# Performance work log

Hardware: AMD Instinct MI355X
Metric: run time of the kernel (lower is better)

## Reference

```python
import jax, jax.numpy as jnp
import numpy as np

B, T, D, H = 4, 2048, 1024, 16
DK, DV, K, I = 48, 96, 4, 3072
EPS = 1e-5


def rmsnorm(x, w, eps=EPS):
    return x * jax.lax.rsqrt(jnp.mean(x * x, -1, keepdims=True) + eps) * w


def l2norm(x, eps=1e-6):
    return x * jax.lax.rsqrt(jnp.sum(x * x, -1, keepdims=True) + eps)


def causal_conv(x, w):
    # x: [B,T,C], w: [C,K]; causal depthwise conv (torch cross-correlation semantics)
    k = w.shape[1]
    xp = jnp.pad(x, ((0, 0), (k - 1, 0), (0, 0))).transpose(0, 2, 1)  # [B,C,T+K-1]
    y = jax.lax.conv_general_dilated(xp, w[:, None, :], (1,), 'VALID',
                                     feature_group_count=w.shape[0])
    return y.transpose(0, 2, 1)


def gated_delta_rule(q, k, v, g, beta):
    # q,k: [B,T,H,DK]  v: [B,T,H,DV]  g,beta: [B,T,H]
    scale = q.shape[-1] ** -0.5
    qT = jnp.moveaxis(q, 1, 0) * scale
    kT = jnp.moveaxis(k, 1, 0)
    vT = jnp.moveaxis(v, 1, 0)
    gT = jnp.moveaxis(g, 1, 0)
    bT = jnp.moveaxis(beta, 1, 0)
    S0 = jnp.zeros((q.shape[0], q.shape[2], q.shape[3], v.shape[3]), q.dtype)

    def step(S, inp):
        q_t, k_t, v_t, g_t, b_t = inp
        S = S * jnp.exp(g_t)[..., None, None]                      # gated decay
        v_new = (v_t - jnp.einsum('bhk,bhkv->bhv', k_t, S)) * b_t[..., None]
        S = S + k_t[..., None] * v_new[..., None, :]               # delta-rule update
        o_t = jnp.einsum('bhk,bhkv->bhv', q_t, S)
        return S, o_t

    _, o = jax.lax.scan(step, S0, (qT, kT, vT, gT, bT))
    return jnp.moveaxis(o, 0, 1)


def setup_inputs() -> dict:
    key = jax.random.key(0)
    ks = jax.random.split(key, 20)
    s = 0.02
    return {
        'hidden_states': jax.random.normal(ks[0], (B, T, D), jnp.float32),
        'norm1_w': jnp.ones((D,), jnp.float32),
        'q_w': jax.random.normal(ks[1], (D, H * DK), jnp.float32) * s,
        'k_w': jax.random.normal(ks[2], (D, H * DK), jnp.float32) * s,
        'v_w': jax.random.normal(ks[3], (D, H * DV), jnp.float32) * s,
        'conv_q_w': jax.random.normal(ks[4], (H * DK, K), jnp.float32) * 0.2,
        'conv_k_w': jax.random.normal(ks[5], (H * DK, K), jnp.float32) * 0.2,
        'conv_v_w': jax.random.normal(ks[6], (H * DV, K), jnp.float32) * 0.2,
        'b_w': jax.random.normal(ks[7], (D, H), jnp.float32) * s,
        'a_w': jax.random.normal(ks[8], (D, H), jnp.float32) * s,
        'A_log': jnp.log(jax.random.uniform(ks[9], (H,), jnp.float32, 1.0, 16.0)),
        'dt_bias': jax.random.normal(ks[10], (H,), jnp.float32) * 0.5,
        'g_w': jax.random.normal(ks[11], (D, H * DV), jnp.float32) * s,
        'o_norm_w': jnp.ones((DV,), jnp.float32),
        'o_w': jax.random.normal(ks[12], (H * DV, D), jnp.float32) * s,
        'norm2_w': jnp.ones((D,), jnp.float32),
        'gate_w': jax.random.normal(ks[13], (D, I), jnp.float32) * s,
        'up_w': jax.random.normal(ks[14], (D, I), jnp.float32) * s,
        'down_w': jax.random.normal(ks[15], (I, D), jnp.float32) * s,
    }


def reference(hidden_states, norm1_w, q_w, k_w, v_w, conv_q_w, conv_k_w, conv_v_w,
              b_w, a_w, A_log, dt_bias, g_w, o_norm_w, o_w, norm2_w,
              gate_w, up_w, down_w):
    x = hidden_states
    h = rmsnorm(x, norm1_w)
    # --- GatedDeltaNet mixer ---
    q = jax.nn.silu(causal_conv(h @ q_w, conv_q_w)).reshape(B, T, H, DK)
    k = jax.nn.silu(causal_conv(h @ k_w, conv_k_w)).reshape(B, T, H, DK)
    v = jax.nn.silu(causal_conv(h @ v_w, conv_v_w)).reshape(B, T, H, DV)
    q, k = l2norm(q), l2norm(k)
    beta = jax.nn.sigmoid(h @ b_w)                                  # [B,T,H]
    g = -jnp.exp(A_log) * jax.nn.softplus(h @ a_w + dt_bias)        # [B,T,H] mamba gate
    o = gated_delta_rule(q, k, v, g, beta)                          # [B,T,H,DV]
    gate = (h @ g_w).reshape(B, T, H, DV)
    o = rmsnorm(o, o_norm_w) * (gate * jax.nn.sigmoid(gate))        # fused gated RMSNorm
    x = x + o.reshape(B, T, H * DV) @ o_w
    # --- SwiGLU MLP ---
    h2 = rmsnorm(x, norm2_w)
    x = x + (jax.nn.silu(h2 @ gate_w) * (h2 @ up_w)) @ down_w
    return x
```

## Files before the change

### kernel.cpp

```cpp
#include <hip/hip_runtime.h>
#include <hip/hip_bf16.h>
#include <math.h>

constexpr int Bn = 4, Tn = 2048, Dn = 1024, Hn = 16, DKn = 48, DVn = 96, In = 3072;
constexpr int BT = Bn * Tn;
constexpr int HDK = Hn * DKn;
constexpr int HDV = Hn * DVn;
constexpr int QKVC = 2 * HDK + HDV;
constexpr int CC = 64;
constexpr int NC = Tn / CC;

using bf16 = __hip_bfloat16;
typedef __attribute__((ext_vector_type(8))) short bf16x8;
typedef __attribute__((ext_vector_type(4))) float f32x4;

constexpr size_t WO_HBF   = 0;
constexpr size_t WO_QKVR  = 16777216;
constexpr size_t WO_OSC   = 16777216;
constexpr size_t WO_ACT   = 16777216;
constexpr size_t WO_A     = 16777216;
constexpr size_t WO_B     = 26214400;
constexpr size_t WO_ST    = 45088768;
constexpr size_t WO_QKVC  = 67108864;
constexpr size_t WO_GATE  = 117440512;
constexpr size_t WO_X1    = 142606336;
constexpr size_t WO_BA    = 176160768;
constexpr size_t WO_GC    = 177209344;
constexpr size_t WO_T     = 177733632;
constexpr size_t WO_UV    = 194510848;
constexpr size_t WO_WB    = 219676672;
constexpr size_t WB_QKVT = 0;
constexpr size_t WB_GT   = 3145728;
constexpr size_t WB_OT   = 4718592;
constexpr size_t WB_GATET= 6291456;
constexpr size_t WB_UPT  = 9437184;
constexpr size_t WB_DOWNT= 12582912;
constexpr size_t WB_ABT  = 15728640;

__device__ __forceinline__ float sigmoidf_(float x) { return 1.f / (1.f + __expf(-x)); }
__device__ __forceinline__ float siluf(float x) { return x * sigmoidf_(x); }

__device__ __forceinline__ void glds16(const void* g, void* l) {
  __builtin_amdgcn_global_load_lds((const __attribute__((address_space(1))) void*)g,
                                   (__attribute__((address_space(3))) void*)l, 16, 0, 0);
}

__device__ __forceinline__ f32x4 mfma16(bf16x8 a, bf16x8 b, f32x4 c) {
  return __builtin_amdgcn_mfma_f32_16x16x32_bf16(a, b, c, 0, 0, 0);
}

__device__ __forceinline__ bf16x8 scale8(bf16x8 a, float s) {
  bf16x8 r;
#pragma unroll
  for (int e = 0; e < 8; e++) {
    float f = __bfloat162float(__ushort_as_bfloat16((unsigned short)a[e])) * s;
    r[e] = (short)__bfloat16_as_ushort(__float2bfloat16(f));
  }
  return r;
}

__device__ __forceinline__ float b2f(short u) {
  return __bfloat162float(__ushort_as_bfloat16((unsigned short)u));
}
__device__ __forceinline__ short f2b(float f) {
  return (short)__bfloat16_as_ushort(__float2bfloat16(f));
}

struct TcastArgs {
  const float* src[10];
  bf16* dst[10];
  int R[10], C[10], gxw[10], t0[10];
};

__global__ void tcast_all(TcastArgs a) {
  __shared__ float t[32][33];
  int bid = blockIdx.x;
  int i = 0;
#pragma unroll
  for (int k = 1; k < 10; k++) if (bid >= a.t0[k]) i = k;
  int lt = bid - a.t0[i];
  int gxw = a.gxw[i];
  int bx = lt % gxw, by = lt / gxw;
  const float* in = a.src[i];
  bf16* out = a.dst[i];
  int R = a.R[i], C = a.C[i];
  int tx = threadIdx.x, ty = threadIdx.y;
  int c0 = bx * 32, r0 = by * 32;
#pragma unroll
  for (int j = 0; j < 4; j++) {
    int r = ty + j * 8;
    float v = (c0 + tx < C) ? in[(size_t)(r0 + r) * C + c0 + tx] : 0.f;
    t[r][tx] = v;
  }
  __syncthreads();
#pragma unroll
  for (int j = 0; j < 4; j++) {
    int cc = ty + j * 8;
    if (c0 + cc < C) out[(size_t)(c0 + cc) * R + r0 + tx] = __float2bfloat16(t[tx][cc]);
  }
}

__global__ void rmsnorm_bf_k(const float* __restrict__ x, const float* __restrict__ w,
                             bf16* __restrict__ y) {
  int row = blockIdx.x;
  const float4* xr = (const float4*)(x + (size_t)row * Dn);
  int tid = threadIdx.x;
  float4 v = xr[tid];
  float ss = v.x * v.x + v.y * v.y + v.z * v.z + v.w * v.w;
  for (int m = 32; m >= 1; m >>= 1) ss += __shfl_xor(ss, m, 64);
  __shared__ float wsum[4];
  if ((tid & 63) == 0) wsum[tid >> 6] = ss;
  __syncthreads();
  ss = wsum[0] + wsum[1] + wsum[2] + wsum[3];
  float rs = rsqrtf(ss * (1.f / Dn) + 1e-5f);
  float4 wv = ((const float4*)w)[tid];
  bf16* yr = y + (size_t)row * Dn + tid * 4;
  yr[0] = __float2bfloat16(v.x * rs * wv.x);
  yr[1] = __float2bfloat16(v.y * rs * wv.y);
  yr[2] = __float2bfloat16(v.z * rs * wv.z);
  yr[3] = __float2bfloat16(v.w * rs * wv.w);
}

#define AS256(bi) (lds + (bi) * 8192)
#define BS256(bi) (lds + 32768 + (bi) * 8192)
#define STAGE256(bi, k0) do { \
    glds16(gA0 + (k0), AS256(bi) + w * 512); \
    glds16(gB0 + (k0), BS256(bi) + w * 512); \
  } while (0)

__global__ __launch_bounds__(1024) void gemm256(
    const bf16* __restrict__ A, const bf16* __restrict__ Bt,
    bf16* __restrict__ C0, bf16* __restrict__ C1,
    int gx, int N, int K, int mode) {
  __shared__ bf16 lds[65536];
  int bid = blockIdx.x;
  int xcd = bid & 7, li = bid >> 3;
  int by = xcd * 4 + li / gx;
  int bx = li % gx;
  int bm = by * 256, bn = bx * 256;
  int tid = threadIdx.x;
  int lane = tid & 63, w = tid >> 6;
  int l15 = lane & 15, lq = lane >> 4;
  int wr = w >> 2, wc = w & 3;
  int arow0 = tid >> 2;
  int srcq = (tid & 3) ^ ((arow0 >> 1) & 3);
  const bf16* gA0 = A + (size_t)(bm + arow0) * K + srcq * 8;
  const bf16* gB0 = Bt + (size_t)(bn + arow0) * K + srcq * 8;
  int slot = lq ^ ((l15 >> 1) & 3);
  f32x4 acc[4][4];
#pragma unroll
  for (int m = 0; m < 4; m++)
#pragma unroll
    for (int n = 0; n < 4; n++) acc[m][n] = (f32x4){0.f, 0.f, 0.f, 0.f};
  int NT = K >> 5;
  STAGE256(0, 0);
  STAGE256(1, 32);
  STAGE256(2, 64);
  for (int t = 0; t < NT; ++t) {
    int b = t & 3;
    if (t <= NT - 3)      { asm volatile("s_waitcnt vmcnt(4)" ::: "memory"); }
    else if (t == NT - 2) { asm volatile("s_waitcnt vmcnt(2)" ::: "memory"); }
    else                  { asm volatile("s_waitcnt vmcnt(0)" ::: "memory"); }
    __builtin_amdgcn_s_barrier();
    bf16x8 af[4], bfr[4];
#pragma unroll
    for (int m = 0; m < 4; m++)
      af[m] = *(const bf16x8*)(AS256(b) + (wr * 64 + m * 16 + l15) * 32 + slot * 8);
#pragma unroll
    for (int n = 0; n < 4; n++)
      bfr[n] = *(const bf16x8*)(BS256(b) + (wc * 64 + n * 16 + l15) * 32 + slot * 8);
    __builtin_amdgcn_s_setprio(1);
#pragma unroll
    for (int m = 0; m < 4; m++)
#pragma unroll
      for (int n = 0; n < 4; n++)
        acc[m][n] = mfma16(af[m], bfr[n], acc[m][n]);
    __builtin_amdgcn_s_setprio(0);
    if (t + 3 < NT) STAGE256((t + 3) & 3, (t + 3) * 32);
  }
  __syncthreads();
  bf16* dst; int ldc, bnl;
  if (bn < 3072) { dst = C0; ldc = 3072; bnl = bn; }
  else           { dst = C1; ldc = 1536; bnl = bn - 3072; }
  bf16* cw = lds + w * 4096;
#pragma unroll
  for (int m = 0; m < 4; m++)
#pragma unroll
    for (int n = 0; n < 4; n++)
#pragma unroll
      for (int i = 0; i < 4; i++) {
        int row_l = m * 16 + lq * 4 + i;
        int col_l = n * 16 + l15;
        cw[row_l * 64 + (col_l ^ ((row_l & 7) << 3))] = __float2bfloat16(acc[m][n][i]);
      }
  __syncthreads();
  int r8 = lane >> 3, cblk = lane & 7;
#pragma unroll
  for (int it = 0; it < 8; it++) {
    int row_l = it * 8 + r8;
    int sblk = cblk ^ (row_l & 7);
    bf16x8 val = *(const bf16x8*)&cw[row_l * 64 + sblk * 8];
    *(bf16x8*)&dst[(size_t)(bm + wr * 64 + row_l) * ldc + bnl + wc * 64 + cblk * 8] = val;
  }
}

__global__ __launch_bounds__(1024) void gemm_mlp(
    const bf16* __restrict__ A, const bf16* __restrict__ Bt,
    bf16* __restrict__ C, int K) {
  __shared__ bf16 lds[65536];
  int bid = blockIdx.x;
  int xcd = bid & 7, li = bid >> 3;
  int by = xcd * 4 + li / 24;
  int bx = li % 24;
  int bm = by * 256, bn = bx * 128;
  int tid = threadIdx.x;
  int lane = tid & 63, w = tid >> 6;
  int l15 = lane & 15, lq = lane >> 4;
  int wr = w >> 2, wc = w & 3;
  int r0 = tid >> 2;
  int srcq = (tid & 3) ^ ((r0 >> 1) & 3);
  const bf16* gA0 = A + (size_t)(bm + r0) * K + srcq * 8;
  int growB = bn + (r0 & 127) + (r0 >> 7) * 3072;
  const bf16* gB0 = Bt + (size_t)growB * K + srcq * 8;
  int slot = lq ^ ((l15 >> 1) & 3);
  f32x4 accg[4][2], accu[4][2];
#pragma unroll
  for (int m = 0; m < 4; m++)
#pragma unroll
    for (int n = 0; n < 2; n++) {
      accg[m][n] = (f32x4){0.f, 0.f, 0.f, 0.f};
      accu[m][n] = (f32x4){0.f, 0.f, 0.f, 0.f};
    }
  int NT = K >> 5;
  STAGE256(0, 0);
  STAGE256(1, 32);
  STAGE256(2, 64);
  for (int t = 0; t < NT; ++t) {
    int b = t & 3;
    if (t <= NT - 3)      { asm volatile("s_waitcnt vmcnt(4)" ::: "memory"); }
    else if (t == NT - 2) { asm volatile("s_waitcnt vmcnt(2)" ::: "memory"); }
    else                  { asm volatile("s_waitcnt vmcnt(0)" ::: "memory"); }
    __builtin_amdgcn_s_barrier();
    bf16x8 af[4], bg[2], bu[2];
#pragma unroll
    for (int m = 0; m < 4; m++)
      af[m] = *(const bf16x8*)(AS256(b) + (wr * 64 + m * 16 + l15) * 32 + slot * 8);
#pragma unroll
    for (int n = 0; n < 2; n++) {
      bg[n] = *(const bf16x8*)(BS256(b) + (wc * 32 + n * 16 + l15) * 32 + slot * 8);
      bu[n] = *(const bf16x8*)(BS256(b) + (128 + wc * 32 + n * 16 + l15) * 32 + slot * 8);
    }
    __builtin_amdgcn_s_setprio(1);
#pragma unroll
    for (int m = 0; m < 4; m++)
#pragma unroll
      for (int n = 0; n < 2; n++) {
        accg[m][n] = mfma16(af[m], bg[n], accg[m][n]);
        accu[m][n] = mfma16(af[m], bu[n], accu[m][n]);
      }
    __builtin_amdgcn_s_setprio(0);
    if (t + 3 < NT) STAGE256((t + 3) & 3, (t + 3) * 32);
  }
  __syncthreads();
  bf16* cw = lds + w * 2048;
#pragma unroll
  for (int m = 0; m < 4; m++)
#pragma unroll
    for (int n = 0; n < 2; n++)
#pragma unroll
      for (int i = 0; i < 4; i++) {
        int row_l = m * 16 + lq * 4 + i;
        int col_l = n * 16 + l15;
        float v = siluf(accg[m][n][i]) * accu[m][n][i];
        cw[row_l * 32 + (col_l ^ ((row_l & 3) << 3))] = __float2bfloat16(v);
      }
  __syncthreads();
  int r16 = lane >> 2, cblk = lane & 3;
#pragma unroll
  for (int it = 0; it < 4; it++) {
    int row_l = it * 16 + r16;
    int sblk = cblk ^ (row_l & 3);
    bf16x8 val = *(const bf16x8*)&cw[row_l * 32 + sblk * 8];
    *(bf16x8*)&C[(size_t)(bm + wr * 64 + row_l) * 3072 + bn + wc * 32 + cblk * 8] = val;
  }
}

__global__ __launch_bounds__(1024) void gemm_mfma(
    const bf16* __restrict__ A, const bf16* __restrict__ Bt,
    void* __restrict__ Cv, const float* __restrict__ res,
    int N, int K, int ldc, int mode, int gx, int gy) {
  __shared__ bf16 As[4][4096];
  __shared__ bf16 Bs[4][4096];
  int bid = blockIdx.x;
  int xcd = bid & 7, li = bid >> 3;
  int by = xcd * (gy >> 3) + li / gx;
  int bx = li % gx;
  int tid = threadIdx.x, lane = tid & 63, w = tid >> 6;
  int bm = by * 128, bn = bx * 128;
  int l15 = lane & 15, lq = lane >> 4;
  int wr = w >> 2, wc = w & 3;
  int r0 = (tid & 511) >> 2;
  int sq = (tid & 3) ^ ((r0 >> 1) & 3);
  const bf16* g0;
  bf16* lb;
  if (w < 8) {
    g0 = A + (size_t)(bm + r0) * K + sq * 8;
    lb = &As[0][w * 512];
  } else {
    int br = bn + r0; if (br >= N) br = 0;
    g0 = Bt + (size_t)br * K + sq * 8;
    lb = &Bs[0][(w - 8) * 512];
  }
#define STAGE128X(bi, k0) glds16(g0 + (k0), lb + (bi) * 4096)
  int slot = lq ^ ((l15 >> 1) & 3);
  f32x4 acc[2][2];
#pragma unroll
  for (int m = 0; m < 2; m++)
#pragma unroll
    for (int n = 0; n < 2; n++) acc[m][n] = (f32x4){0.f, 0.f, 0.f, 0.f};
  int NT = K >> 5;
  STAGE128X(0, 0);
  STAGE128X(1, 32);
  STAGE128X(2, 64);
  for (int t = 0; t < NT; ++t) {
    int b = t & 3;
    if (t <= NT - 3)      { asm volatile("s_waitcnt vmcnt(2)" ::: "memory"); }
    else if (t == NT - 2) { asm volatile("s_waitcnt vmcnt(1)" ::: "memory"); }
    else                  { asm volatile("s_waitcnt vmcnt(0)" ::: "memory"); }
    __builtin_amdgcn_s_barrier();
    bf16x8 af[2], bfr[2];
#pragma unroll
    for (int m = 0; m < 2; m++)
      af[m] = *(const bf16x8*)&As[b][(wr * 32 + m * 16 + l15) * 32 + slot * 8];
#pragma unroll
    for (int n = 0; n < 2; n++)
      bfr[n] = *(const bf16x8*)&Bs[b][(wc * 32 + n * 16 + l15) * 32 + slot * 8];
    __builtin_amdgcn_s_setprio(1);
#pragma unroll
    for (int m = 0; m < 2; m++)
#pragma unroll
      for (int n = 0; n < 2; n++)
        acc[m][n] = mfma16(af[m], bfr[n], acc[m][n]);
    __builtin_amdgcn_s_setprio(0);
    if (t + 3 < NT) STAGE128X((t + 3) & 3, (t + 3) * 32);
  }
#pragma unroll
  for (int m = 0; m < 2; m++) {
#pragma unroll
    for (int n = 0; n < 2; n++) {
      int col = bn + wc * 32 + n * 16 + l15;
      if (col >= N) continue;
#pragma unroll
      for (int i = 0; i < 4; i++) {
        int row = bm + wr * 32 + m * 16 + lq * 4 + i;
        float v = acc[m][n][i];
        size_t idx = (size_t)row * ldc + col;
        if (mode == 0) {
          if (res) v += res[idx];
          ((float*)Cv)[idx] = v;
        } else {
          ((bf16*)Cv)[idx] = __float2bfloat16(v);
        }
      }
    }
  }
}

__global__ __launch_bounds__(256) void convsilu2_k(const bf16* __restrict__ in,
                                                   bf16* __restrict__ outp,
                                                   const float* __restrict__ wq,
                                                   const float* __restrict__ wk,
                                                   const float* __restrict__ wv) {
  int tx = threadIdx.x & 31;
  int ty = threadIdx.x >> 5;
  int c = (blockIdx.x * 32 + tx) * 8;
  int gt = blockIdx.y * 8 + ty;
  int b = gt >> 11, t = gt & (Tn - 1);
  const float* wsrc = (c < HDK) ? (wq + c * 4)
                     : (c < 2 * HDK) ? (wk + (c - HDK) * 4)
                                     : (wv + (c - 2 * HDK) * 4);
  float4 W[8];
#pragma unroll
  for (int j = 0; j < 8; j++) W[j] = ((const float4*)wsrc)[j];
  const bf16* base = in + (size_t)b * Tn * QKVC + c;
  bf16x8 r[4];
  bf16x8 zero = {0, 0, 0, 0, 0, 0, 0, 0};
#pragma unroll
  for (int j = 0; j < 4; j++) {
    int tt = t - 3 + j;
    r[j] = (tt >= 0) ? *(const bf16x8*)(base + (size_t)tt * QKVC) : zero;
  }
  bf16x8 o;
#pragma unroll
  for (int ch = 0; ch < 8; ch++) {
    float x0 = b2f(r[0][ch]), x1 = b2f(r[1][ch]), x2 = b2f(r[2][ch]), x3 = b2f(r[3][ch]);
    float y = x0 * W[ch].x + x1 * W[ch].y + x2 * W[ch].z + x3 * W[ch].w;
    o[ch] = f2b(siluf(y));
  }
  *(bf16x8*)(outp + (size_t)gt * QKVC + c) = o;
}

__global__ __launch_bounds__(256) void l2norm_k(bf16* __restrict__ qkv) {
  int row = blockIdx.x * 256 + threadIdx.x;
  int t = row >> 5, hr = row & 31;
  bf16* p = qkv + (size_t)t * QKVC + hr * DKn;
  bf16x8 v[6];
  float ss = 0.f;
#pragma unroll
  for (int j = 0; j < 6; j++) {
    v[j] = *(const bf16x8*)(p + j * 8);
#pragma unroll
    for (int e = 0; e < 8; e++) { float f = b2f(v[j][e]); ss += f * f; }
  }
  float rs = rsqrtf(ss + 1e-6f);
#pragma unroll
  for (int j = 0; j < 6; j++) {
    bf16x8 o;
#pragma unroll
    for (int e = 0; e < 8; e++) o[e] = f2b(b2f(v[j][e]) * rs);
    *(bf16x8*)(p + j * 8) = o;
  }
}

__global__ void betag_k(float* __restrict__ ba, const float* __restrict__ A_log,
                        const float* __restrict__ dt_bias) {
  int i = blockIdx.x * blockDim.x + threadIdx.x;
  int h = i & 15, r = i >> 4;
  float bv = ba[(size_t)r * 32 + h];
  float av = ba[(size_t)r * 32 + 16 + h];
  ba[(size_t)r * 32 + h] = sigmoidf_(bv);
  float xx = av + dt_bias[h];
  float sp = (xx > 20.f) ? xx : log1pf(__expf(xx));
  ba[(size_t)r * 32 + 16 + h] = -__expf(A_log[h]) * sp;
}

__global__ __launch_bounds__(256) void dn_p1a(const bf16* __restrict__ qkv,
                                              const float* __restrict__ ba,
                                              float* __restrict__ Gc_g,
                                              bf16* __restrict__ T_g,
                                              bf16* __restrict__ Uv_g,
                                              bf16* __restrict__ A_g,
                                              bf16* __restrict__ B_g) {
  __shared__ __align__(16) char smem[62976];
  bf16 (*Kl)[72]   = (bf16(*)[72])(smem);
  bf16 (*Tl)[72]   = (bf16(*)[72])(smem + 9216);
  bf16 (*UvdT)[72] = (bf16(*)[72])(smem + 18432);
  float* Gcl = (float*)(smem + 32256);
  float* Bl  = (float*)(smem + 32512);
  bf16 (*Vl)[100]  = (bf16(*)[100])(smem + 32768);
  float (*Nl)[68]  = (float(*)[68])(smem + 45568);
  bf16 (*KTl)[72]  = (bf16(*)[72])(smem + 32768);
  bf16 (*KTbl)[72] = (bf16(*)[72])(smem + 39680);
  bf16 (*M2T)[72]  = (bf16(*)[72])(smem + 46592);
  int cid = blockIdx.x;
  int nc = cid & (NC - 1);
  int bh = cid >> 5;
  int h = bh & 15, b = bh >> 4;
  int t0 = nc * CC;
  int tid = threadIdx.x, lane = tid & 63, w = tid >> 6;
  int l15 = lane & 15, qd = lane >> 4;
  bf16 zb = __float2bfloat16(0.f);
  {
    int t = tid >> 2, p = tid & 3;
    const bf16* row = qkv + ((size_t)(b * Tn + t0 + t)) * QKVC;
    int c0 = p * 12;
#pragma unroll
    for (int j = 0; j < 12; ++j) Kl[t][c0 + j] = row[HDK + h * DKn + c0 + j];
    int j0 = p * 24;
#pragma unroll
    for (int j = 0; j < 24; ++j) Vl[t][j0 + j] = row[2 * HDK + h * DVn + j0 + j];
  }
  for (int i = tid; i < 64 * 24; i += 256) {
    int t = i / 24, c = 48 + (i % 24);
    Kl[t][c] = zb;
  }
  if (tid < 64) {
    size_t row = (size_t)(b * Tn + t0 + tid);
    float g = ba[row * 32 + 16 + h];
    float be = ba[row * 32 + h];
    float acc = g;
#pragma unroll
    for (int d = 1; d < 64; d <<= 1) {
      float o = __shfl_up(acc, d);
      if (tid >= d) acc += o;
    }
    Gcl[tid] = acc; Bl[tid] = be;
    Gc_g[(size_t)bh * Tn + t0 + tid] = acc;
  }
  __syncthreads();
  f32x4 dacc[4];
#pragma unroll
  for (int n = 0; n < 4; n++) dacc[n] = (f32x4){0.f, 0.f, 0.f, 0.f};
  {
    int arow = w * 16 + l15;
    bf16x8 a0 = *(const bf16x8*)&Kl[arow][qd * 8];
    bf16x8 a1 = *(const bf16x8*)&Kl[arow][32 + qd * 8];
#pragma unroll
    for (int n = 0; n < 4; n++) {
      int brow = n * 16 + l15;
      bf16x8 b0 = *(const bf16x8*)&Kl[brow][qd * 8];
      bf16x8 b1 = *(const bf16x8*)&Kl[brow][32 + qd * 8];
      dacc[n] = mfma16(a0, b0, dacc[n]);
      dacc[n] = mfma16(a1, b1, dacc[n]);
    }
  }
#pragma unroll
  for (int i = 0; i < 4; i++) {
    int t = w * 16 + qd * 4 + i;
    float bt = Bl[t], gt = Gcl[t];
#pragma unroll
    for (int n = 0; n < 4; n++) {
      int s = n * 16 + l15;
      Nl[t][s] = (s < t) ? bt * __expf(gt - Gcl[s]) * dacc[n][i] : 0.f;
    }
  }
  __syncthreads();
  float g63 = Gcl[63];
  int c = tid;
  if (c < 160) {
    float R[64];
    if (c < 64) {
#pragma unroll
      for (int t = 0; t < 64; ++t) R[t] = (t == c) ? 1.f : 0.f;
    } else {
      int j = c - 64;
#pragma unroll
      for (int t = 0; t < 64; ++t) R[t] = Bl[t] * __bfloat162float(Vl[t][j]);
    }
#pragma unroll
    for (int t = 1; t < 64; ++t) {
      float a0 = 0.f, a1 = 0.f, a2 = 0.f, a3 = 0.f;
#pragma unroll
      for (int s = 0; s + 3 < t; s += 4) {
        float4 n4 = *(const float4*)&Nl[t][s];
        a0 += n4.x * R[s]; a1 += n4.y * R[s + 1];
        a2 += n4.z * R[s + 2]; a3 += n4.w * R[s + 3];
      }
#pragma unroll
      for (int s = t & ~3; s < t; ++s) a0 += Nl[t][s] * R[s];
      R[t] -= ((a0 + a1) + (a2 + a3));
    }
    if (c < 64) {
#pragma unroll
      for (int t = 0; t < 64; ++t) {
        bf16 v = __float2bfloat16(R[t]);
        T_g[(size_t)cid * 4096 + t * 64 + c] = v;
        Tl[t][c] = v;
      }
    } else {
      int j = c - 64;
#pragma unroll
      for (int t = 0; t < 64; ++t) {
        Uv_g[(size_t)cid * 6144 + t * 96 + j] = __float2bfloat16(R[t]);
        UvdT[j][t] = __float2bfloat16(R[t] * __expf(g63 - Gcl[t]));
      }
    }
  }
  __syncthreads();
  for (int i = tid; i < 48 * 64; i += 256) {
    int dk = i >> 6, t = i & 63;
    bf16 kv = Kl[t][dk];
    KTl[dk][t] = kv;
    float bl = Bl[t] * __expf(Gcl[t]);
    KTbl[dk][t] = __float2bfloat16(__bfloat162float(kv) * bl);
  }
  __syncthreads();
  f32x4 m1[3];
#pragma unroll
  for (int n = 0; n < 3; n++) m1[n] = (f32x4){0.f, 0.f, 0.f, 0.f};
  {
    int arow = w * 16 + l15;
    bf16x8 a0 = *(const bf16x8*)&Tl[arow][qd * 8];
    bf16x8 a1 = *(const bf16x8*)&Tl[arow][32 + qd * 8];
#pragma unroll
    for (int n = 0; n < 3; n++) {
      int brow = n * 16 + l15;
      bf16x8 b0 = *(const bf16x8*)&KTbl[brow][qd * 8];
      bf16x8 b1 = *(const bf16x8*)&KTbl[brow][32 + qd * 8];
      m1[n] = mfma16(a0, b0, m1[n]);
      m1[n] = mfma16(a1, b1, m1[n]);
    }
  }
#pragma unroll
  for (int i = 0; i < 4; i++) {
    int tt = w * 16 + qd * 4 + i;
    float dd = __expf(g63 - Gcl[tt]);
#pragma unroll
    for (int n = 0; n < 3; n++) {
      int dk = n * 16 + l15;
      M2T[dk][tt] = __float2bfloat16(m1[n][i] * dd);
    }
  }
  __syncthreads();
  float lamC = __expf(g63);
#pragma unroll
  for (int tswap = 0; tswap < 7; tswap++) {
    int t = w + 4 * tswap;
    if (t >= 27) break;
    int mi, ni; bool isA;
    if (t < 9) { isA = true; mi = t / 3; ni = t % 3; }
    else { isA = false; mi = (t - 9) / 6; ni = (t - 9) % 6; }
    f32x4 acc = (f32x4){0.f, 0.f, 0.f, 0.f};
    int arow = mi * 16 + l15;
    bf16x8 a0 = *(const bf16x8*)&KTl[arow][qd * 8];
    bf16x8 a1 = *(const bf16x8*)&KTl[arow][32 + qd * 8];
    int brow = ni * 16 + l15;
    if (isA) {
      bf16x8 b0 = *(const bf16x8*)&M2T[brow][qd * 8];
      bf16x8 b1 = *(const bf16x8*)&M2T[brow][32 + qd * 8];
      acc = mfma16(a0, b0, acc);
      acc = mfma16(a1, b1, acc);
#pragma unroll
      for (int i = 0; i < 4; i++) {
        int row = mi * 16 + qd * 4 + i, colv = ni * 16 + l15;
        float v = ((row == colv) ? lamC : 0.f) - acc[i];
        A_g[(size_t)cid * 2304 + row * 48 + colv] = __float2bfloat16(v);
      }
    } else {
      bf16x8 b0 = *(const bf16x8*)&UvdT[brow][qd * 8];
      bf16x8 b1 = *(const bf16x8*)&UvdT[brow][32 + qd * 8];
      acc = mfma16(a0, b0, acc);
      acc = mfma16(a1, b1, acc);
#pragma unroll
      for (int i = 0; i < 4; i++) {
        int row = mi * 16 + qd * 4 + i, colv = ni * 16 + l15;
        B_g[(size_t)cid * 4608 + row * 96 + colv] = __float2bfloat16(acc[i]);
      }
    }
  }
}

__global__ __launch_bounds__(256) void dn_p2b(const bf16* __restrict__ A_g,
                                              const bf16* __restrict__ B_g,
                                              bf16* __restrict__ St_g) {
  __shared__ bf16 STl[2][96][72];
  __shared__ bf16 Al[2][48][72];
  __shared__ bf16 Bl[2][4608];
  int bh = blockIdx.x;
  int tid = threadIdx.x, lane = tid & 63, w = tid >> 6;
  int l15 = lane & 15, qd = lane >> 4;
  bf16 zb = __float2bfloat16(0.f);
  for (int i = tid; i < 2 * 96 * 72; i += 256) (&STl[0][0][0])[i] = zb;
  for (int i = tid; i < 2 * 48 * 24; i += 256) {
    int buf = i / (48 * 24), r = (i / 24) % 48, cc = 48 + (i % 24);
    Al[buf][r][cc] = zb;
  }
  bf16x8 ra0, ra1, rb0, rb1;
  unsigned int rb2;
  int e_a0 = tid * 8, e_a1 = 2048 + tid * 8;
  {
    size_t cid = (size_t)bh * NC;
    ra0 = *(const bf16x8*)(A_g + cid * 2304 + e_a0);
    if (tid < 32) ra1 = *(const bf16x8*)(A_g + cid * 2304 + e_a1);
    rb0 = *(const bf16x8*)(B_g + cid * 4608 + tid * 16);
    rb1 = *(const bf16x8*)(B_g + cid * 4608 + tid * 16 + 8);
    rb2 = *(const unsigned int*)(B_g + cid * 4608 + 4096 + tid * 2);
  }
  *(bf16x8*)&Al[0][e_a0 / 48][e_a0 % 48] = ra0;
  if (tid < 32) *(bf16x8*)&Al[0][e_a1 / 48][e_a1 % 48] = ra1;
  *(bf16x8*)&Bl[0][tid * 16] = rb0;
  *(bf16x8*)&Bl[0][tid * 16 + 8] = rb1;
  *(unsigned int*)&Bl[0][4096 + tid * 2] = rb2;
  {
    size_t cid = (size_t)bh * NC + 1;
    ra0 = *(const bf16x8*)(A_g + cid * 2304 + e_a0);
    if (tid < 32) ra1 = *(const bf16x8*)(A_g + cid * 2304 + e_a1);
    rb0 = *(const bf16x8*)(B_g + cid * 4608 + tid * 16);
    rb1 = *(const bf16x8*)(B_g + cid * 4608 + tid * 16 + 8);
    rb2 = *(const unsigned int*)(B_g + cid * 4608 + 4096 + tid * 2);
  }
  __syncthreads();

  for (int c = 0; c < NC - 1; ++c) {
    int cur = c & 1, nxt = cur ^ 1;
    size_t cid = (size_t)bh * NC + c;
    {
      int e0 = tid * 8, e1 = 2048 + tid * 8, e2 = 4096 + tid * 2;
      *(bf16x8*)(St_g + cid * 4608 + e0) = *(const bf16x8*)&STl[cur][e0 / 48][e0 % 48];
      *(bf16x8*)(St_g + cid * 4608 + e1) = *(const bf16x8*)&STl[cur][e1 / 48][e1 % 48];
      *(unsigned int*)(St_g + cid * 4608 + e2) = *(const unsigned int*)&STl[cur][e2 / 48][e2 % 48];
    }
    float vals[5][4];
#pragma unroll
    for (int ts = 0; ts < 5; ts++) {
      int t = w + 4 * ts;
      if (t >= 18) break;
      int mi = t / 3, ni = t % 3;
      f32x4 acc = (f32x4){0.f, 0.f, 0.f, 0.f};
      int arow = mi * 16 + l15;
      bf16x8 a0 = *(const bf16x8*)&STl[cur][arow][qd * 8];
      bf16x8 a1 = *(const bf16x8*)&STl[cur][arow][32 + qd * 8];
      int brow = ni * 16 + l15;
      bf16x8 b0 = *(const bf16x8*)&Al[cur][brow][qd * 8];
      bf16x8 b1 = *(const bf16x8*)&Al[cur][brow][32 + qd * 8];
      acc = mfma16(a0, b0, acc);
      acc = mfma16(a1, b1, acc);
#pragma unroll
      for (int i = 0; i < 4; i++) {
        int dv = mi * 16 + qd * 4 + i, ii = ni * 16 + l15;
        vals[ts][i] = acc[i] + __bfloat162float(Bl[cur][ii * 96 + dv]);
      }
    }
#pragma unroll
    for (int ts = 0; ts < 5; ts++) {
      int t = w + 4 * ts;
      if (t >= 18) break;
      int mi = t / 3, ni = t % 3;
#pragma unroll
      for (int i = 0; i < 4; i++) {
        int dv = mi * 16 + qd * 4 + i, ii = ni * 16 + l15;
        STl[nxt][dv][ii] = __float2bfloat16(vals[ts][i]);
      }
    }
    if (c + 1 <= NC - 2) {
      *(bf16x8*)&Al[nxt][e_a0 / 48][e_a0 % 48] = ra0;
      if (tid < 32) *(bf16x8*)&Al[nxt][e_a1 / 48][e_a1 % 48] = ra1;
      *(bf16x8*)&Bl[nxt][tid * 16] = rb0;
      *(bf16x8*)&Bl[nxt][tid * 16 + 8] = rb1;
      *(unsigned int*)&Bl[nxt][4096 + tid * 2] = rb2;
      if (c + 2 <= NC - 2) {
        size_t cid2 = (size_t)bh * NC + c + 2;
        ra0 = *(const bf16x8*)(A_g + cid2 * 2304 + e_a0);
        if (tid < 32) ra1 = *(const bf16x8*)(A_g + cid2 * 2304 + e_a1);
        rb0 = *(const bf16x8*)(B_g + cid2 * 4608 + tid * 16);
        rb1 = *(const bf16x8*)(B_g + cid2 * 4608 + tid * 16 + 8);
        rb2 = *(const unsigned int*)(B_g + cid2 * 4608 + 4096 + tid * 2);
      }
    }
    __syncthreads();
  }
  {
    size_t cid = (size_t)bh * NC + (NC - 1);
    int cur = (NC - 1) & 1;
    int e0 = tid * 8, e1 = 2048 + tid * 8, e2 = 4096 + tid * 2;
    *(bf16x8*)(St_g + cid * 4608 + e0) = *(const bf16x8*)&STl[cur][e0 / 48][e0 % 48];
    *(bf16x8*)(St_g + cid * 4608 + e1) = *(const bf16x8*)&STl[cur][e1 / 48][e1 % 48];
    *(unsigned int*)(St_g + cid * 4608 + e2) = *(const unsigned int*)&STl[cur][e2 / 48][e2 % 48];
  }
}

__global__ __launch_bounds__(256) void dn_p2c(const bf16* __restrict__ qkv,
                                              const float* __restrict__ ba,
                                              const float* __restrict__ Gc_g,
                                              const bf16* __restrict__ T_g,
                                              const bf16* __restrict__ Uv_g,
                                              const bf16* __restrict__ St_g,
                                              const bf16* __restrict__ gate,
                                              const float* __restrict__ onw,
                                              bf16* __restrict__ attn) {
  __shared__ bf16 Kl[64][72], Ql[64][72], Tl[64][72], Ml[64][72];
  __shared__ bf16 G1T[96][72], UT[96][72], STb[96][72];
  __shared__ float Gcl[64], Bl[64];
  __shared__ float onwl[96];
  int cid = blockIdx.x;
  int nc = cid & (NC - 1);
  int bh = cid >> 5;
  int h = bh & 15, b = bh >> 4;
  int t0 = nc * CC;
  int tid = threadIdx.x, lane = tid & 63, w = tid >> 6;
  int l15 = lane & 15, qd = lane >> 4;
  const float scale = 0.14433756729740643f;
  bf16 zb = __float2bfloat16(0.f);
  {
    int t = tid >> 2, p = tid & 3;
    size_t grow = (size_t)(b * Tn + t0 + t);
    const bf16* row = qkv + grow * QKVC;
    int c0 = p * 12;
#pragma unroll
    for (int j = 0; j < 12; ++j) {
      int cc = c0 + j;
      Kl[t][cc] = row[HDK + h * DKn + cc];
      Ql[t][cc] = __float2bfloat16(__bfloat162float(row[h * DKn + cc]) * scale);
    }
    if (p == 0) { Gcl[t] = Gc_g[(size_t)bh * Tn + t0 + t]; Bl[t] = ba[grow * 32 + h]; }
  }
  if (tid < 96) onwl[tid] = onw[tid];
  for (int i = tid; i < 64 * 16; i += 256) {
    int t = i >> 4, cc = 48 + (i & 15);
    Kl[t][cc] = zb; Ql[t][cc] = zb;
  }
  for (int i = tid; i < 4096; i += 256)
    (&Tl[0][0])[(i >> 6) * 72 + (i & 63)] = T_g[(size_t)cid * 4096 + i];
  for (int i = tid; i < 4608; i += 256)
    STb[i / 48][i % 48] = St_g[(size_t)cid * 4608 + i];
  for (int i = tid; i < 96 * 16; i += 256)
    STb[i >> 4][48 + (i & 15)] = zb;
  __syncthreads();
  f32x4 acc[6];
#pragma unroll
  for (int n = 0; n < 6; n++) acc[n] = (f32x4){0.f, 0.f, 0.f, 0.f};
  {
    int arow = w * 16 + l15;
    bf16x8 a0 = *(const bf16x8*)&Kl[arow][qd * 8];
    bf16x8 a1 = *(const bf16x8*)&Kl[arow][32 + qd * 8];
#pragma unroll
    for (int n = 0; n < 6; n++) {
      int brow = n * 16 + l15;
      bf16x8 b0 = *(const bf16x8*)&STb[brow][qd * 8];
      bf16x8 b1 = *(const bf16x8*)&STb[brow][32 + qd * 8];
      acc[n] = mfma16(a0, b0, acc[n]);
      acc[n] = mfma16(a1, b1, acc[n]);
    }
  }
#pragma unroll
  for (int i = 0; i < 4; i++) {
    int tt = w * 16 + qd * 4 + i;
    float sc = Bl[tt] * __expf(Gcl[tt]);
#pragma unroll
    for (int n = 0; n < 6; n++)
      G1T[n * 16 + l15][tt] = __float2bfloat16(acc[n][i] * sc);
  }
  __syncthreads();
#pragma unroll
  for (int n = 0; n < 6; n++) acc[n] = (f32x4){0.f, 0.f, 0.f, 0.f};
  {
    int arow = w * 16 + l15;
    bf16x8 a0 = *(const bf16x8*)&Tl[arow][qd * 8];
    bf16x8 a1 = *(const bf16x8*)&Tl[arow][32 + qd * 8];
#pragma unroll
    for (int n = 0; n < 6; n++) {
      int brow = n * 16 + l15;
      bf16x8 b0 = *(const bf16x8*)&G1T[brow][qd * 8];
      bf16x8 b1 = *(const bf16x8*)&G1T[brow][32 + qd * 8];
      acc[n] = mfma16(a0, b0, acc[n]);
      acc[n] = mfma16(a1, b1, acc[n]);
    }
  }
#pragma unroll
  for (int i = 0; i < 4; i++) {
    int tt = w * 16 + qd * 4 + i;
#pragma unroll
    for (int n = 0; n < 6; n++) {
      int dv = n * 16 + l15;
      float uv = __bfloat162float(Uv_g[(size_t)cid * 6144 + tt * 96 + dv]);
      UT[dv][tt] = __float2bfloat16(uv - acc[n][i]);
    }
  }
  f32x4 qk[4];
#pragma unroll
  for (int n = 0; n < 4; n++) qk[n] = (f32x4){0.f, 0.f, 0.f, 0.f};
  {
    int arow = w * 16 + l15;
    bf16x8 a0 = *(const bf16x8*)&Ql[arow][qd * 8];
    bf16x8 a1 = *(const bf16x8*)&Ql[arow][32 + qd * 8];
#pragma unroll
    for (int n = 0; n < 4; n++) {
      int brow = n * 16 + l15;
      bf16x8 b0 = *(const bf16x8*)&Kl[brow][qd * 8];
      bf16x8 b1 = *(const bf16x8*)&Kl[brow][32 + qd * 8];
      qk[n] = mfma16(a0, b0, qk[n]);
      qk[n] = mfma16(a1, b1, qk[n]);
    }
  }
#pragma unroll
  for (int i = 0; i < 4; i++) {
    int tt = w * 16 + qd * 4 + i;
    float gt = Gcl[tt];
#pragma unroll
    for (int n = 0; n < 4; n++) {
      int ss = n * 16 + l15;
      float m = (ss <= tt) ? qk[n][i] * __expf(gt - Gcl[ss]) : 0.f;
      Ml[tt][ss] = __float2bfloat16(m);
    }
  }
  __syncthreads();
#pragma unroll
  for (int n = 0; n < 6; n++) acc[n] = (f32x4){0.f, 0.f, 0.f, 0.f};
  {
    int arow = w * 16 + l15;
    float lam = __expf(Gcl[arow]);
    bf16x8 a0 = scale8(*(const bf16x8*)&Ql[arow][qd * 8], lam);
    bf16x8 a1 = scale8(*(const bf16x8*)&Ql[arow][32 + qd * 8], lam);
    bf16x8 m0 = *(const bf16x8*)&Ml[arow][qd * 8];
    bf16x8 m1 = *(const bf16x8*)&Ml[arow][32 + qd * 8];
#pragma unroll
    for (int n = 0; n < 6; n++) {
      int brow = n * 16 + l15;
      bf16x8 b0 = *(const bf16x8*)&STb[brow][qd * 8];
      bf16x8 b1 = *(const bf16x8*)&STb[brow][32 + qd * 8];
      acc[n] = mfma16(a0, b0, acc[n]);
      acc[n] = mfma16(a1, b1, acc[n]);
      bf16x8 u0 = *(const bf16x8*)&UT[brow][qd * 8];
      bf16x8 u1 = *(const bf16x8*)&UT[brow][32 + qd * 8];
      acc[n] = mfma16(m0, u0, acc[n]);
      acc[n] = mfma16(m1, u1, acc[n]);
    }
  }
#pragma unroll
  for (int i = 0; i < 4; i++) {
    int tt = w * 16 + qd * 4 + i;
    float ss = 0.f;
#pragma unroll
    for (int n = 0; n < 6; n++) ss += acc[n][i] * acc[n][i];
    ss += __shfl_xor(ss, 1, 64);
    ss += __shfl_xor(ss, 2, 64);
    ss += __shfl_xor(ss, 4, 64);
    ss += __shfl_xor(ss, 8, 64);
    float rs = rsqrtf(ss * (1.f / DVn) + 1e-5f);
    size_t orow = ((size_t)(b * Tn + t0 + tt)) * HDV + h * DVn;
#pragma unroll
    for (int n = 0; n < 6; n++) {
      int dv = n * 16 + l15;
      float g = __bfloat162float(gate[orow + dv]);
      attn[orow + dv] = __float2bfloat16(acc[n][i] * rs * onwl[dv] * siluf(g));
    }
  }
}

extern "C" void kernel_launch(void* const* d_in, const int* in_sizes, int n_in,
                              void* d_out, int out_size, void* d_ws, size_t ws_size,
                              hipStream_t stream) {
  const float* x       = (const float*)d_in[0];
  const float* norm1_w = (const float*)d_in[1];
  const float* q_w     = (const float*)d_in[2];
  const float* k_w     = (const float*)d_in[3];
  const float* v_w     = (const float*)d_in[4];
  const float* cq_w    = (const float*)d_in[5];
  const float* ck_w    = (const float*)d_in[6];
  const float* cv_w    = (const float*)d_in[7];
  const float* b_w     = (const float*)d_in[8];
  const float* a_w     = (const float*)d_in[9];
  const float* A_log   = (const float*)d_in[10];
  const float* dt_bias = (const float*)d_in[11];
  const float* g_w     = (const float*)d_in[12];
  const float* o_norm_w= (const float*)d_in[13];
  const float* o_w     = (const float*)d_in[14];
  const float* norm2_w = (const float*)d_in[15];
  const float* gate_w  = (const float*)d_in[16];
  const float* up_w    = (const float*)d_in[17];
  const float* down_w  = (const float*)d_in[18];
  char* wsb = (char*)d_ws;
  float* out = (float*)d_out;

  bf16*  hbf   = (bf16*)(wsb + WO_HBF);
  bf16*  qkvr  = (bf16*)(wsb + WO_QKVR);
  bf16*  qkvc  = (bf16*)(wsb + WO_QKVC);
  bf16*  attn  = (bf16*)(wsb + WO_OSC);
  bf16*  actb  = (bf16*)(wsb + WO_ACT);
  bf16*  gateb = (bf16*)(wsb + WO_GATE);
  float* x1    = (float*)(wsb + WO_X1);
  float* ba    = (float*)(wsb + WO_BA);
  float* Gc    = (float*)(wsb + WO_GC);
  bf16*  Tg    = (bf16*)(wsb + WO_T);
  bf16*  Uvg   = (bf16*)(wsb + WO_UV);
  bf16*  A_g   = (bf16*)(wsb + WO_A);
  bf16*  B_g   = (bf16*)(wsb + WO_B);
  bf16*  St_g  = (bf16*)(wsb + WO_ST);
  bf16*  wb    = (bf16*)(wsb + WO_WB);

  {
    TcastArgs ta;
    const float* srcs[10] = {q_w, k_w, v_w, g_w, o_w, gate_w, up_w, down_w, b_w, a_w};
    bf16* dsts[10] = {wb + WB_QKVT, wb + WB_QKVT + 768 * 1024, wb + WB_QKVT + 1536 * 1024,
                      wb + WB_GT, wb + WB_OT, wb + WB_GATET, wb + WB_UPT, wb + WB_DOWNT,
                      wb + WB_ABT, wb + WB_ABT + 16 * 1024};
    int Rs[10] = {1024, 1024, 1024, 1024, 1536, 1024, 1024, 3072, 1024, 1024};
    int Cs[10] = {768, 768, 1536, 1536, 1024, 3072, 3072, 1024, 16, 16};
    int off = 0;
    for (int i = 0; i < 10; i++) {
      ta.src[i] = srcs[i]; ta.dst[i] = dsts[i];
      ta.R[i] = Rs[i]; ta.C[i] = Cs[i];
      ta.gxw[i] = (Cs[i] + 31) / 32;
      ta.t0[i] = off;
      off += ta.gxw[i] * (Rs[i] / 32);
    }
    tcast_all<<<off, dim3(32, 8), 0, stream>>>(ta);
  }

  rmsnorm_bf_k<<<BT, 256, 0, stream>>>(x, norm1_w, hbf);
  gemm256<<<576, 1024, 0, stream>>>(hbf, wb + WB_QKVT, qkvr, gateb, 18, 4608, 1024, 10);
  gemm_mfma<<<64, 1024, 0, stream>>>(hbf, wb + WB_ABT, ba, nullptr, 32, 1024, 32, 0, 1, 64);
  convsilu2_k<<<dim3(QKVC / 256, BT / 8), 256, 0, stream>>>(qkvr, qkvc, cq_w, ck_w, cv_w);
  l2norm_k<<<(BT * 32) / 256, 256, 0, stream>>>(qkvc);
  betag_k<<<(BT * Hn) / 256, 256, 0, stream>>>(ba, A_log, dt_bias);
  dn_p1a<<<Bn * Hn * NC, 256, 0, stream>>>(qkvc, ba, Gc, Tg, Uvg, A_g, B_g);
  dn_p2b<<<Bn * Hn, 256, 0, stream>>>(A_g, B_g, St_g);
  dn_p2c<<<Bn * Hn * NC, 256, 0, stream>>>(qkvc, ba, Gc, Tg, Uvg, St_g, gateb, o_norm_w, attn);
  gemm_mfma<<<512, 1024, 0, stream>>>(attn, wb + WB_OT, x1, x, 1024, 1536, 1024, 0, 8, 64);
  rmsnorm_bf_k<<<BT, 256, 0, stream>>>(x1, norm2_w, hbf);
  gemm_mlp<<<768, 1024, 0, stream>>>(hbf, wb + WB_GATET, actb, 1024);
  gemm_mfma<<<512, 1024, 0, stream>>>(actb, wb + WB_DOWNT, out, x1, 1024, 3072, 1024, 0, 8, 64);
}
```

Measured before the change: 587.5 us.

## Fuse conv+l2norm for q/k, split state scan over DV, remap GEMM tiles

```diff
diff --git a/kernel.cpp b/kernel.cpp
--- a/kernel.cpp
+++ b/kernel.cpp
@@ -135,8 +135,8 @@
   __shared__ bf16 lds[65536];
   int bid = blockIdx.x;
   int xcd = bid & 7, li = bid >> 3;
-  int by = xcd * 4 + li / gx;
-  int bx = li % gx;
+  int by = xcd * 4 + (li & 3);
+  int bx = li >> 2;
   int bm = by * 256, bn = bx * 256;
   int tid = threadIdx.x;
   int lane = tid & 63, w = tid >> 6;
@@ -210,8 +210,8 @@
   __shared__ bf16 lds[65536];
   int bid = blockIdx.x;
   int xcd = bid & 7, li = bid >> 3;
-  int by = xcd * 4 + li / 24;
-  int bx = li % 24;
+  int by = xcd * 4 + (li & 3);
+  int bx = li >> 2;
   int bm = by * 256, bn = bx * 128;
   int tid = threadIdx.x;
   int lane = tid & 63, w = tid >> 6;
@@ -293,8 +293,9 @@
   __shared__ bf16 Bs[4][4096];
   int bid = blockIdx.x;
   int xcd = bid & 7, li = bid >> 3;
-  int by = xcd * (gy >> 3) + li / gx;
-  int bx = li % gx;
+  int bpg = gy >> 3;
+  int by = xcd * bpg + li % bpg;
+  int bx = li / bpg;
   int tid = threadIdx.x, lane = tid & 63, w = tid >> 6;
   int bm = by * 128, bn = bx * 128;
   int l15 = lane & 15, lq = lane >> 4;
@@ -370,10 +371,11 @@
                                                    bf16* __restrict__ outp,
                                                    const float* __restrict__ wq,
                                                    const float* __restrict__ wk,
-                                                   const float* __restrict__ wv) {
+                                                   const float* __restrict__ wv,
+                                                   int coff) {
   int tx = threadIdx.x & 31;
   int ty = threadIdx.x >> 5;
-  int c = (blockIdx.x * 32 + tx) * 8;
+  int c = (blockIdx.x * 32 + tx) * 8 + coff;
   int gt = blockIdx.y * 8 + ty;
   int b = gt >> 11, t = gt & (Tn - 1);
   const float* wsrc = (c < HDK) ? (wq + c * 4)
@@ -400,25 +402,50 @@
   *(bf16x8*)(outp + (size_t)gt * QKVC + c) = o;
 }
 
-__global__ __launch_bounds__(256) void l2norm_k(bf16* __restrict__ qkv) {
+__global__ __launch_bounds__(256) void convl2_k(const bf16* __restrict__ in,
+                                                bf16* __restrict__ outp,
+                                                const float* __restrict__ wq,
+                                                const float* __restrict__ wk) {
   int row = blockIdx.x * 256 + threadIdx.x;
-  int t = row >> 5, hr = row & 31;
-  bf16* p = qkv + (size_t)t * QKVC + hr * DKn;
-  bf16x8 v[6];
+  int gt = row >> 5, hr = row & 31;
+  int b = gt >> 11, t = gt & (Tn - 1);
+  int ch0 = hr * DKn;
+  const float* wbase = (hr < 16) ? (wq + ch0 * 4) : (wk + (ch0 - HDK) * 4);
+  const bf16* base = in + (size_t)b * Tn * QKVC + ch0;
+  bf16x8 zero = {0, 0, 0, 0, 0, 0, 0, 0};
+  bf16x8 outv[6];
   float ss = 0.f;
 #pragma unroll
   for (int j = 0; j < 6; j++) {
-    v[j] = *(const bf16x8*)(p + j * 8);
-#pragma unroll
-    for (int e = 0; e < 8; e++) { float f = b2f(v[j][e]); ss += f * f; }
+    float4 W[8];
+#pragma unroll
+    for (int e = 0; e < 8; e++) W[e] = ((const float4*)wbase)[j * 8 + e];
+    bf16x8 r[4];
+#pragma unroll
+    for (int k = 0; k < 4; k++) {
+      int tt = t - 3 + k;
+      r[k] = (tt >= 0) ? *(const bf16x8*)(base + (size_t)tt * QKVC + j * 8) : zero;
+    }
+    bf16x8 o;
+#pragma unroll
+    for (int e = 0; e < 8; e++) {
+      float y = b2f(r[0][e]) * W[e].x + b2f(r[1][e]) * W[e].y +
+                b2f(r[2][e]) * W[e].z + b2f(r[3][e]) * W[e].w;
+      short bs = f2b(siluf(y));
+      float sv = b2f(bs);
+      ss += sv * sv;
+      o[e] = bs;
+    }
+    outv[j] = o;
   }
   float rs = rsqrtf(ss + 1e-6f);
+  bf16* op = outp + (size_t)gt * QKVC + ch0;
 #pragma unroll
   for (int j = 0; j < 6; j++) {
     bf16x8 o;
 #pragma unroll
-    for (int e = 0; e < 8; e++) o[e] = f2b(b2f(v[j][e]) * rs);
-    *(bf16x8*)(p + j * 8) = o;
+    for (int e = 0; e < 8; e++) o[e] = f2b(b2f(outv[j][e]) * rs);
+    *(bf16x8*)(op + j * 8) = o;
   }
 }
 
@@ -633,41 +660,38 @@
 __global__ __launch_bounds__(256) void dn_p2b(const bf16* __restrict__ A_g,
                                               const bf16* __restrict__ B_g,
                                               bf16* __restrict__ St_g) {
-  __shared__ bf16 STl[2][96][72];
+  __shared__ bf16 STl[2][48][72];
   __shared__ bf16 Al[2][48][72];
-  __shared__ bf16 Bl[2][4608];
-  int bh = blockIdx.x;
+  __shared__ bf16 Bl[2][2304];
+  int bh = blockIdx.x >> 1;
+  int dv0 = (blockIdx.x & 1) * 48;
   int tid = threadIdx.x, lane = tid & 63, w = tid >> 6;
   int l15 = lane & 15, qd = lane >> 4;
   bf16 zb = __float2bfloat16(0.f);
-  for (int i = tid; i < 2 * 96 * 72; i += 256) (&STl[0][0][0])[i] = zb;
+  for (int i = tid; i < 2 * 48 * 72; i += 256) (&STl[0][0][0])[i] = zb;
   for (int i = tid; i < 2 * 48 * 24; i += 256) {
     int buf = i / (48 * 24), r = (i / 24) % 48, cc = 48 + (i % 24);
     Al[buf][r][cc] = zb;
   }
   bf16x8 ra0, ra1, rb0, rb1;
-  unsigned int rb2;
   int e_a0 = tid * 8, e_a1 = 2048 + tid * 8;
   {
     size_t cid = (size_t)bh * NC;
     ra0 = *(const bf16x8*)(A_g + cid * 2304 + e_a0);
     if (tid < 32) ra1 = *(const bf16x8*)(A_g + cid * 2304 + e_a1);
-    rb0 = *(const bf16x8*)(B_g + cid * 4608 + tid * 16);
-    rb1 = *(const bf16x8*)(B_g + cid * 4608 + tid * 16 + 8);
-    rb2 = *(const unsigned int*)(B_g + cid * 4608 + 4096 + tid * 2);
+    rb0 = *(const bf16x8*)(B_g + cid * 4608 + (e_a0 / 48) * 96 + dv0 + (e_a0 % 48));
+    if (tid < 32) rb1 = *(const bf16x8*)(B_g + cid * 4608 + (e_a1 / 48) * 96 + dv0 + (e_a1 % 48));
   }
   *(bf16x8*)&Al[0][e_a0 / 48][e_a0 % 48] = ra0;
   if (tid < 32) *(bf16x8*)&Al[0][e_a1 / 48][e_a1 % 48] = ra1;
-  *(bf16x8*)&Bl[0][tid * 16] = rb0;
-  *(bf16x8*)&Bl[0][tid * 16 + 8] = rb1;
-  *(unsigned int*)&Bl[0][4096 + tid * 2] = rb2;
+  *(bf16x8*)&Bl[0][e_a0] = rb0;
+  if (tid < 32) *(bf16x8*)&Bl[0][e_a1] = rb1;
   {
     size_t cid = (size_t)bh * NC + 1;
     ra0 = *(const bf16x8*)(A_g + cid * 2304 + e_a0);
     if (tid < 32) ra1 = *(const bf16x8*)(A_g + cid * 2304 + e_a1);
-    rb0 = *(const bf16x8*)(B_g + cid * 4608 + tid * 16);
-    rb1 = *(const bf16x8*)(B_g + cid * 4608 + tid * 16 + 8);
-    rb2 = *(const unsigned int*)(B_g + cid * 4608 + 4096 + tid * 2);
+    rb0 = *(const bf16x8*)(B_g + cid * 4608 + (e_a0 / 48) * 96 + dv0 + (e_a0 % 48));
+    if (tid < 32) rb1 = *(const bf16x8*)(B_g + cid * 4608 + (e_a1 / 48) * 96 + dv0 + (e_a1 % 48));
   }
   __syncthreads();
 
@@ -675,16 +699,16 @@
     int cur = c & 1, nxt = cur ^ 1;
     size_t cid = (size_t)bh * NC + c;
     {
-      int e0 = tid * 8, e1 = 2048 + tid * 8, e2 = 4096 + tid * 2;
-      *(bf16x8*)(St_g + cid * 4608 + e0) = *(const bf16x8*)&STl[cur][e0 / 48][e0 % 48];
-      *(bf16x8*)(St_g + cid * 4608 + e1) = *(const bf16x8*)&STl[cur][e1 / 48][e1 % 48];
-      *(unsigned int*)(St_g + cid * 4608 + e2) = *(const unsigned int*)&STl[cur][e2 / 48][e2 % 48];
-    }
-    float vals[5][4];
-#pragma unroll
-    for (int ts = 0; ts < 5; ts++) {
+      size_t sb = cid * 4608 + (size_t)dv0 * 48;
+      *(bf16x8*)(St_g + sb + e_a0) = *(const bf16x8*)&STl[cur][e_a0 / 48][e_a0 % 48];
+      if (tid < 32)
+        *(bf16x8*)(St_g + sb + e_a1) = *(const bf16x8*)&STl[cur][e_a1 / 48][e_a1 % 48];
+    }
+    float vals[3][4];
+#pragma unroll
+    for (int ts = 0; ts < 3; ts++) {
       int t = w + 4 * ts;
-      if (t >= 18) break;
+      if (t >= 9) break;
       int mi = t / 3, ni = t % 3;
       f32x4 acc = (f32x4){0.f, 0.f, 0.f, 0.f};
       int arow = mi * 16 + l15;
@@ -697,34 +721,32 @@
       acc = mfma16(a1, b1, acc);
 #pragma unroll
       for (int i = 0; i < 4; i++) {
-        int dv = mi * 16 + qd * 4 + i, ii = ni * 16 + l15;
-        vals[ts][i] = acc[i] + __bfloat162float(Bl[cur][ii * 96 + dv]);
-      }
-    }
-#pragma unroll
-    for (int ts = 0; ts < 5; ts++) {
+        int dvl = mi * 16 + qd * 4 + i, ii = ni * 16 + l15;
+        vals[ts][i] = acc[i] + __bfloat162float(Bl[cur][ii * 48 + dvl]);
+      }
+    }
+#pragma unroll
+    for (int ts = 0; ts < 3; ts++) {
       int t = w + 4 * ts;
-      if (t >= 18) break;
+      if (t >= 9) break;
       int mi = t / 3, ni = t % 3;
 #pragma unroll
       for (int i = 0; i < 4; i++) {
-        int dv = mi * 16 + qd * 4 + i, ii = ni * 16 + l15;
-        STl[nxt][dv][ii] = __float2bfloat16(vals[ts][i]);
+        int dvl = mi * 16 + qd * 4 + i, ii = ni * 16 + l15;
+        STl[nxt][dvl][ii] = __float2bfloat16(vals[ts][i]);
       }
     }
     if (c + 1 <= NC - 2) {
       *(bf16x8*)&Al[nxt][e_a0 / 48][e_a0 % 48] = ra0;
       if (tid < 32) *(bf16x8*)&Al[nxt][e_a1 / 48][e_a1 % 48] = ra1;
-      *(bf16x8*)&Bl[nxt][tid * 16] = rb0;
-      *(bf16x8*)&Bl[nxt][tid * 16 + 8] = rb1;
-      *(unsigned int*)&Bl[nxt][4096 + tid * 2] = rb2;
+      *(bf16x8*)&Bl[nxt][e_a0] = rb0;
+      if (tid < 32) *(bf16x8*)&Bl[nxt][e_a1] = rb1;
       if (c + 2 <= NC - 2) {
         size_t cid2 = (size_t)bh * NC + c + 2;
         ra0 = *(const bf16x8*)(A_g + cid2 * 2304 + e_a0);
         if (tid < 32) ra1 = *(const bf16x8*)(A_g + cid2 * 2304 + e_a1);
-        rb0 = *(const bf16x8*)(B_g + cid2 * 4608 + tid * 16);
-        rb1 = *(const bf16x8*)(B_g + cid2 * 4608 + tid * 16 + 8);
-        rb2 = *(const unsigned int*)(B_g + cid2 * 4608 + 4096 + tid * 2);
+        rb0 = *(const bf16x8*)(B_g + cid2 * 4608 + (e_a0 / 48) * 96 + dv0 + (e_a0 % 48));
+        if (tid < 32) rb1 = *(const bf16x8*)(B_g + cid2 * 4608 + (e_a1 / 48) * 96 + dv0 + (e_a1 % 48));
       }
     }
     __syncthreads();
@@ -732,10 +754,10 @@
   {
     size_t cid = (size_t)bh * NC + (NC - 1);
     int cur = (NC - 1) & 1;
-    int e0 = tid * 8, e1 = 2048 + tid * 8, e2 = 4096 + tid * 2;
-    *(bf16x8*)(St_g + cid * 4608 + e0) = *(const bf16x8*)&STl[cur][e0 / 48][e0 % 48];
-    *(bf16x8*)(St_g + cid * 4608 + e1) = *(const bf16x8*)&STl[cur][e1 / 48][e1 % 48];
-    *(unsigned int*)(St_g + cid * 4608 + e2) = *(const unsigned int*)&STl[cur][e2 / 48][e2 % 48];
+    size_t sb = cid * 4608 + (size_t)dv0 * 48;
+    *(bf16x8*)(St_g + sb + e_a0) = *(const bf16x8*)&STl[cur][e_a0 / 48][e_a0 % 48];
+    if (tid < 32)
+      *(bf16x8*)(St_g + sb + e_a1) = *(const bf16x8*)&STl[cur][e_a1 / 48][e_a1 % 48];
   }
 }
 
@@ -970,11 +992,11 @@
   rmsnorm_bf_k<<<BT, 256, 0, stream>>>(x, norm1_w, hbf);
   gemm256<<<576, 1024, 0, stream>>>(hbf, wb + WB_QKVT, qkvr, gateb, 18, 4608, 1024, 10);
   gemm_mfma<<<64, 1024, 0, stream>>>(hbf, wb + WB_ABT, ba, nullptr, 32, 1024, 32, 0, 1, 64);
-  convsilu2_k<<<dim3(QKVC / 256, BT / 8), 256, 0, stream>>>(qkvr, qkvc, cq_w, ck_w, cv_w);
-  l2norm_k<<<(BT * 32) / 256, 256, 0, stream>>>(qkvc);
+  convl2_k<<<(BT * 32) / 256, 256, 0, stream>>>(qkvr, qkvc, cq_w, ck_w);
+  convsilu2_k<<<dim3(6, BT / 8), 256, 0, stream>>>(qkvr, qkvc, cq_w, ck_w, cv_w, 2 * HDK);
   betag_k<<<(BT * Hn) / 256, 256, 0, stream>>>(ba, A_log, dt_bias);
   dn_p1a<<<Bn * Hn * NC, 256, 0, stream>>>(qkvc, ba, Gc, Tg, Uvg, A_g, B_g);
-  dn_p2b<<<Bn * Hn, 256, 0, stream>>>(A_g, B_g, St_g);
+  dn_p2b<<<Bn * Hn * 2, 256, 0, stream>>>(A_g, B_g, St_g);
   dn_p2c<<<Bn * Hn * NC, 256, 0, stream>>>(qkvc, ba, Gc, Tg, Uvg, St_g, gateb, o_norm_w, attn);
   gemm_mfma<<<512, 1024, 0, stream>>>(attn, wb + WB_OT, x1, x, 1024, 1536, 1024, 0, 8, 64);
   rmsnorm_bf_k<<<BT, 256, 0, stream>>>(x1, norm2_w, hbf);
```

Measured after the change: 597.1 us. Within noise of the previous version (+1.6%).
